# Kernel optimization log

Hardware: AMD Instinct MI355X
Metric: run time of the kernel (lower is better)

Reference implementation:

```python
import jax, jax.numpy as jnp
import numpy as np

N, E, F_IN = 50000, 800000, 128
H, C, CLS, G = 8, 32, 16, 64
NEG_SLOPE = 0.2


def setup_inputs() -> dict:
    key = jax.random.key(0)
    ks = jax.random.split(key, 11)
    s = 0.05
    return {
        "x": jax.random.normal(ks[0], (N, F_IN), jnp.float32),
        "edge_index": jax.random.randint(ks[1], (2, E), 0, N, jnp.int32),
        "batch": jnp.sort(jax.random.randint(ks[2], (N,), 0, G, jnp.int32)),
        "W1": jax.random.normal(ks[3], (F_IN, H * C), jnp.float32) * s,
        "a1_src": jax.random.normal(ks[4], (H, C), jnp.float32) * s,
        "a1_dst": jax.random.normal(ks[5], (H, C), jnp.float32) * s,
        "b1": jax.random.normal(ks[6], (H * C,), jnp.float32) * s,
        "W2": jax.random.normal(ks[7], (H * C, CLS), jnp.float32) * s,
        "a2_src": jax.random.normal(ks[8], (1, CLS), jnp.float32) * s,
        "a2_dst": jax.random.normal(ks[9], (1, CLS), jnp.float32) * s,
        "b2": jax.random.normal(ks[10], (CLS,), jnp.float32) * s,
    }


def _gat_conv(x, src, dst, W, a_s, a_d, b, concat):
    n = x.shape[0]
    Hh, Cc = a_s.shape
    xp = (x @ W).reshape(n, Hh, Cc)                      # [N,H,C]
    al_s = jnp.einsum("nhc,hc->nh", xp, a_s)             # [N,H]
    al_d = jnp.einsum("nhc,hc->nh", xp, a_d)
    e = jax.nn.leaky_relu(al_s[src] + al_d[dst], NEG_SLOPE)  # [E,H]
    m = jax.ops.segment_max(e, dst, num_segments=n)      # segment softmax over dst
    ex = jnp.exp(e - m[dst])
    denom = jax.ops.segment_sum(ex, dst, num_segments=n)
    alpha = ex / denom[dst]                              # [E,H]
    out = jax.ops.segment_sum(xp[src] * alpha[:, :, None], dst, num_segments=n)
    out = out.reshape(n, Hh * Cc) if concat else out.mean(axis=1)
    return out + b


def reference(x, edge_index, batch, W1, a1_src, a1_dst, b1, W2, a2_src, a2_dst, b2):
    n = x.shape[0]
    loops = jnp.arange(n, dtype=edge_index.dtype)        # PyG add_self_loops=True
    ei = jnp.concatenate([edge_index, jnp.stack([loops, loops])], axis=1)
    src, dst = ei[0], ei[1]
    h = jax.nn.elu(_gat_conv(x, src, dst, W1, a1_src, a1_dst, b1, True))
    h = _gat_conv(h, src, dst, W2, a2_src, a2_dst, b2, False)
    counts = jax.ops.segment_sum(jnp.ones((n,), h.dtype), batch, num_segments=G)
    pooled = jax.ops.segment_sum(h, batch, num_segments=G) / jnp.maximum(counts, 1.0)[:, None]
    return jax.nn.log_softmax(pooled, axis=1)
```

## Files before the change

kernel.cpp:

```cpp
#include <hip/hip_runtime.h>
#include <math.h>

#define N_NODES 50000
#define N_EDGES 800000
#define FDIM 128
#define NH 8
#define NC 32
#define D1 256
#define NCLS 16
#define NGRP 64
#define NEG 0.2f
#define E_TOT (N_EDGES + N_NODES)
#define NB_N 196
#define G1_BLOCKS 782
#define E_CHUNK 4096
#define NCHUNK 196
#define NBIN 196

typedef __attribute__((ext_vector_type(8))) unsigned short u16x8;
typedef __attribute__((ext_vector_type(4))) unsigned short u16x4;
typedef __attribute__((ext_vector_type(8))) short short8;
typedef __attribute__((ext_vector_type(4))) float f32x4;

static __device__ __forceinline__ float bf2f(unsigned short u) {
    return __uint_as_float(((unsigned int)u) << 16);
}
static __device__ __forceinline__ unsigned short f2bf(float f) {
    unsigned int b = __float_as_uint(f);
    return (unsigned short)((b + 0x7FFFu + ((b >> 16) & 1u)) >> 16);
}

__global__ __launch_bounds__(256) void k_init(
    const float* __restrict__ W1, unsigned short* __restrict__ w1p,
    float* __restrict__ poolS, float* __restrict__ poolC,
    const int* __restrict__ ei, int* __restrict__ binmat) {
    __shared__ int h[NBIN];
    int c = blockIdx.x;
    for (int b = threadIdx.x; b < NBIN; b += 256) h[b] = 0;
    __syncthreads();
    int e0 = c * E_CHUNK;
    int e1 = e0 + E_CHUNK; if (e1 > N_EDGES) e1 = N_EDGES;
    for (int e = e0 + threadIdx.x; e < e1; e += 256)
        atomicAdd(&h[ei[N_EDGES + e] >> 8], 1);
    int i = blockIdx.x * 256 + threadIdx.x;
    if (i < NGRP * NCLS) poolS[i] = 0.f;
    if (i < NGRP) poolC[i] = 0.f;
    if (i < FDIM * D1) {
        int ks = i >> 13;
        int r = i & 8191;
        int nt2 = r >> 9;
        int r2 = r & 511;
        int lane = r2 >> 3, e = r2 & 7;
        int k = ks * 32 + (lane >> 4) * 8 + e;
        int col = nt2 * 16 + (lane & 15);
        w1p[i] = f2bf(W1[k * D1 + col]);
    }
    __syncthreads();
    for (int b = threadIdx.x; b < NBIN; b += 256) binmat[b * NCHUNK + c] = h[b];
}

__global__ __launch_bounds__(256) void k_binprescan(int* __restrict__ binmat,
                                                    int* __restrict__ binTot) {
    __shared__ int sh[256];
    int b = blockIdx.x, t = threadIdx.x;
    int v = (t < NCHUNK) ? binmat[b * NCHUNK + t] : 0;
    sh[t] = v;
    __syncthreads();
    for (int d = 1; d < 256; d <<= 1) {
        int tv = (t >= d) ? sh[t - d] : 0;
        __syncthreads();
        sh[t] += tv;
        __syncthreads();
    }
    if (t < NCHUNK) binmat[b * NCHUNK + t] = sh[t] - v;
    if (t == 255) binTot[b] = sh[255];
}

__global__ __launch_bounds__(256) void k_basescan(const int* __restrict__ binTot,
                                                  int* __restrict__ binBase) {
    __shared__ int sh[256];
    int t = threadIdx.x;
    int v = (t < NBIN) ? binTot[t] : 0;
    sh[t] = v;
    __syncthreads();
    for (int d = 1; d < 256; d <<= 1) {
        int tv = (t >= d) ? sh[t - d] : 0;
        __syncthreads();
        sh[t] += tv;
        __syncthreads();
    }
    if (t < NBIN) binBase[t] = sh[t] - v;
}

__global__ __launch_bounds__(256) void k_gemm1m(
    const float* __restrict__ x, const unsigned short* __restrict__ w1p,
    const float* __restrict__ a1s, const float* __restrict__ a1d,
    unsigned short* __restrict__ xp1b, float* __restrict__ al1s,
    float* __restrict__ al1d) {
    const int l = threadIdx.x & 63;
    const int wid = threadIdx.x >> 6;
    const int wr = wid >> 1, wc = wid & 1;
    const int l15 = l & 15, l4 = l >> 4;
    const int base = blockIdx.x * 64;
    const int r0 = base + wr * 32;

    f32x4 acc[2][8] = {};
#pragma unroll
    for (int ks = 0; ks < 4; ++ks) {
        const int kk = ks * 32 + l4 * 8;
        short8 af[2];
#pragma unroll
        for (int rt = 0; rt < 2; ++rt) {
            int row = r0 + rt * 16 + l15;
            float4 v0 = make_float4(0.f, 0.f, 0.f, 0.f), v1 = v0;
            if (row < N_NODES) {
                const float* xr = x + (size_t)row * FDIM + kk;
                v0 = *(const float4*)xr;
                v1 = *(const float4*)(xr + 4);
            }
            short8 a;
            a[0] = (short)f2bf(v0.x); a[1] = (short)f2bf(v0.y);
            a[2] = (short)f2bf(v0.z); a[3] = (short)f2bf(v0.w);
            a[4] = (short)f2bf(v1.x); a[5] = (short)f2bf(v1.y);
            a[6] = (short)f2bf(v1.z); a[7] = (short)f2bf(v1.w);
            af[rt] = a;
        }
#pragma unroll
        for (int nt = 0; nt < 8; ++nt) {
            int nt2 = wc * 8 + nt;
            short8 bf_ = *(const short8*)&w1p[(size_t)((ks * 16 + nt2) * 64 + l) * 8];
            acc[0][nt] = __builtin_amdgcn_mfma_f32_16x16x32_bf16(af[0], bf_, acc[0][nt], 0, 0, 0);
            acc[1][nt] = __builtin_amdgcn_mfma_f32_16x16x32_bf16(af[1], bf_, acc[1][nt], 0, 0, 0);
        }
    }
#pragma unroll
    for (int rt = 0; rt < 2; ++rt) {
        int rbase = r0 + rt * 16 + l4 * 4;
#pragma unroll
        for (int nt = 0; nt < 8; ++nt) {
            int col = wc * 128 + nt * 16 + l15;
            f32x4 c = acc[rt][nt];
#pragma unroll
            for (int r = 0; r < 4; ++r) {
                int row = rbase + r;
                if (row < N_NODES) xp1b[(size_t)row * D1 + col] = f2bf(c[r]);
            }
        }
    }
#pragma unroll
    for (int hl = 0; hl < 4; ++hl) {
        int hg = wc * 4 + hl;
        float as0 = a1s[hg * NC + l15], as1 = a1s[hg * NC + 16 + l15];
        float ad0 = a1d[hg * NC + l15], ad1 = a1d[hg * NC + 16 + l15];
#pragma unroll
        for (int rt = 0; rt < 2; ++rt) {
            f32x4 c0 = acc[rt][2 * hl], c1 = acc[rt][2 * hl + 1];
#pragma unroll
            for (int r = 0; r < 4; ++r) {
                float ss = c0[r] * as0 + c1[r] * as1;
                float dd = c0[r] * ad0 + c1[r] * ad1;
#pragma unroll
                for (int msk = 1; msk < 16; msk <<= 1) {
                    ss += __shfl_xor(ss, msk);
                    dd += __shfl_xor(dd, msk);
                }
                int row = r0 + rt * 16 + l4 * 4 + r;
                if (l15 == 0 && row < N_NODES) {
                    al1s[row * NH + hg] = ss;
                    al1d[row * NH + hg] = dd;
                }
            }
        }
    }
}

__global__ __launch_bounds__(256) void k_binscatter(const int* __restrict__ ei,
                                                    const int* __restrict__ offs,
                                                    const int* __restrict__ binBase,
                                                    int* __restrict__ binned) {
    __shared__ int cur[NBIN];
    int c = blockIdx.x;
    for (int b = threadIdx.x; b < NBIN; b += 256)
        cur[b] = binBase[b] + offs[b * NCHUNK + c];
    __syncthreads();
    int e0 = c * E_CHUNK;
    int e1 = e0 + E_CHUNK; if (e1 > N_EDGES) e1 = N_EDGES;
    for (int e = e0 + threadIdx.x; e < e1; e += 256) {
        int s = ei[e], d = ei[N_EDGES + e];
        int pos = atomicAdd(&cur[d >> 8], 1);
        binned[pos] = s | ((d & 255) << 16);
    }
}

__global__ __launch_bounds__(256) void k_bincsr(const int* __restrict__ binBase,
                                                const int* __restrict__ binned,
                                                int* __restrict__ rowptr,
                                                int* __restrict__ cnt,
                                                int* __restrict__ esrc) {
    __shared__ int lcnt[256];
    __shared__ int sh[256];
    __shared__ int lcur[256];
    int b = blockIdx.x;
    int t = threadIdx.x;
    int estart = binBase[b];
    int eend = (b == NBIN - 1) ? N_EDGES : binBase[b + 1];
    int nbase = b * 256;
    int nin = N_NODES - nbase; if (nin > 256) nin = 256;
    lcnt[t] = 0;
    __syncthreads();
    for (int e = estart + t; e < eend; e += 256)
        atomicAdd(&lcnt[(binned[e] >> 16) & 255], 1);
    __syncthreads();
    int myc = lcnt[t] + (t < nin ? 1 : 0);
    sh[t] = myc;
    __syncthreads();
    for (int d = 1; d < 256; d <<= 1) {
        int v = (t >= d) ? sh[t - d] : 0;
        __syncthreads();
        sh[t] += v;
        __syncthreads();
    }
    int excl = sh[t] - myc;
    int outbase = estart + nbase;
    int rp = outbase + excl;
    if (t < nin) {
        rowptr[nbase + t] = rp;
        cnt[nbase + t] = myc;
        esrc[rp] = nbase + t;
    }
    lcur[t] = rp + (t < nin ? 1 : 0);
    __syncthreads();
    for (int e = estart + t; e < eend; e += 256) {
        int v = binned[e];
        int pos = atomicAdd(&lcur[(v >> 16) & 255], 1);
        esrc[pos] = v & 0xFFFF;
    }
}

__global__ __launch_bounds__(256) void k_att1(
    const unsigned short* __restrict__ xp1b, const float* __restrict__ al1s,
    const float* __restrict__ al1d, const float* __restrict__ b1,
    const int* __restrict__ rowptr, const int* __restrict__ cnt,
    const int* __restrict__ esrc, unsigned short* __restrict__ h1b) {
    __shared__ int s_src[4][64];
    __shared__ float s_alpha[4][64 * 8];
    int wv = threadIdx.x >> 6;
    int lane = threadIdx.x & 63;
    int n = blockIdx.x * 4 + wv;
    int start = rowptr[n];
    int deg = cnt[n];
    int dcap = deg < 64 ? deg : 64;
    for (int j = lane; j < dcap; j += 64) s_src[wv][j] = esrc[start + j];
    int h = lane & 7, eg = lane >> 3;
    float ald = al1d[n * NH + h];
    float m = -1e30f, den = 0.f;
    for (int j = eg; j < dcap; j += 8) {
        int s = s_src[wv][j];
        float v = al1s[s * NH + h] + ald;
        v = v > 0.f ? v : NEG * v;
        s_alpha[wv][j * 8 + h] = v;
        if (v > m) { den = den * __expf(m - v) + 1.f; m = v; }
        else den += __expf(v - m);
    }
    for (int j = 64 + eg; j < deg; j += 8) {
        int s = esrc[start + j];
        float v = al1s[s * NH + h] + ald;
        v = v > 0.f ? v : NEG * v;
        if (v > m) { den = den * __expf(m - v) + 1.f; m = v; }
        else den += __expf(v - m);
    }
    for (int msk = 8; msk < 64; msk <<= 1) {
        float mo = __shfl_xor(m, msk), dn = __shfl_xor(den, msk);
        float nm = fmaxf(m, mo);
        den = den * __expf(m - nm) + dn * __expf(mo - nm);
        m = nm;
    }
    float rden1 = 1.f / den;
    for (int j = eg; j < dcap; j += 8) {
        float v = s_alpha[wv][j * 8 + h];
        s_alpha[wv][j * 8 + h] = __expf(v - m) * rden1;
    }
    int hh = lane >> 3;
    int cb = lane << 2;
    float m2 = __shfl(m, hh);
    float rd2 = __shfl(rden1, hh);
    float ald2 = al1d[n * NH + hh];
    float a0 = 0.f, a1 = 0.f, a2 = 0.f, a3 = 0.f;
    for (int j0 = 0; j0 < dcap; j0 += 8) {
        const unsigned short* p[8];
        float aw[8];
#pragma unroll
        for (int k = 0; k < 8; ++k) {
            int e = j0 + k;
            bool act = e < dcap;
            int ee = act ? e : 0;
            int s = s_src[wv][ee];
            aw[k] = act ? s_alpha[wv][ee * 8 + hh] : 0.f;
            p[k] = xp1b + (size_t)s * D1 + cb;
        }
#pragma unroll
        for (int k = 0; k < 8; ++k) {
            u16x4 xv = *(const u16x4*)p[k];
            a0 = fmaf(aw[k], bf2f(xv[0]), a0);
            a1 = fmaf(aw[k], bf2f(xv[1]), a1);
            a2 = fmaf(aw[k], bf2f(xv[2]), a2);
            a3 = fmaf(aw[k], bf2f(xv[3]), a3);
        }
    }
    for (int j = 64; j < deg; ++j) {
        int s = esrc[start + j];
        float v = al1s[s * NH + hh] + ald2;
        v = v > 0.f ? v : NEG * v;
        float al = __expf(v - m2) * rd2;
        u16x4 xv = *(const u16x4*)(xp1b + (size_t)s * D1 + cb);
        a0 = fmaf(al, bf2f(xv[0]), a0);
        a1 = fmaf(al, bf2f(xv[1]), a1);
        a2 = fmaf(al, bf2f(xv[2]), a2);
        a3 = fmaf(al, bf2f(xv[3]), a3);
    }
    float4 bb = *(const float4*)(b1 + cb);
    a0 += bb.x; a1 += bb.y; a2 += bb.z; a3 += bb.w;
    a0 = a0 > 0.f ? a0 : expm1f(a0);
    a1 = a1 > 0.f ? a1 : expm1f(a1);
    a2 = a2 > 0.f ? a2 : expm1f(a2);
    a3 = a3 > 0.f ? a3 : expm1f(a3);
    u16x4 pk = { f2bf(a0), f2bf(a1), f2bf(a2), f2bf(a3) };
    *(u16x4*)(h1b + (size_t)n * D1 + cb) = pk;
}

__global__ __launch_bounds__(256) void k_gemm2(
    const unsigned short* __restrict__ h1b, const float* __restrict__ W2,
    const float* __restrict__ a2s, const float* __restrict__ a2d,
    float* __restrict__ xp2, float* __restrict__ al2s, float* __restrict__ al2d) {
    __shared__ float w2s[D1 * NCLS];
    for (int i = threadIdx.x; i < D1 * NCLS; i += 256) w2s[i] = W2[i];
    __syncthreads();
    int n = blockIdx.x * 256 + threadIdx.x;
    if (n >= N_NODES) return;
    float4 acc[4];
#pragma unroll
    for (int q = 0; q < 4; ++q) acc[q] = make_float4(0.f, 0.f, 0.f, 0.f);
    const unsigned short* hr = h1b + (size_t)n * D1;
    for (int k0 = 0; k0 < D1; k0 += 8) {
        u16x8 hv = *(const u16x8*)(hr + k0);
#pragma unroll
        for (int j = 0; j < 8; ++j) {
            float hx = bf2f(hv[j]);
#pragma unroll
            for (int q = 0; q < 4; ++q) {
                float4 w = *(const float4*)(&w2s[(k0 + j) * NCLS + q * 4]);
                acc[q].x = fmaf(hx, w.x, acc[q].x);
                acc[q].y = fmaf(hx, w.y, acc[q].y);
                acc[q].z = fmaf(hx, w.z, acc[q].z);
                acc[q].w = fmaf(hx, w.w, acc[q].w);
            }
        }
    }
    float ss = 0.f, dd = 0.f;
#pragma unroll
    for (int q = 0; q < 4; ++q) {
        *(float4*)(xp2 + (size_t)n * NCLS + q * 4) = acc[q];
        float4 s4 = *(const float4*)(a2s + q * 4);
        float4 d4 = *(const float4*)(a2d + q * 4);
        ss += acc[q].x * s4.x + acc[q].y * s4.y + acc[q].z * s4.z + acc[q].w * s4.w;
        dd += acc[q].x * d4.x + acc[q].y * d4.y + acc[q].z * d4.z + acc[q].w * d4.w;
    }
    al2s[n] = ss;
    al2d[n] = dd;
}

__global__ __launch_bounds__(256) void k_att2(
    const float* __restrict__ xp2, const float* __restrict__ al2s,
    const float* __restrict__ al2d, const float* __restrict__ b2,
    const int* __restrict__ rowptr, const int* __restrict__ cnt,
    const int* __restrict__ esrc, float* __restrict__ out2) {
    __shared__ int s_src[4][64];
    __shared__ float s_a[4][64];
    int wave = threadIdx.x >> 6;
    int lane = threadIdx.x & 63;
    int n = blockIdx.x * 4 + wave;
    int start = rowptr[n];
    int deg = cnt[n];
    int dcap = deg < 64 ? deg : 64;
    float ald = al2d[n];
    float m = -1e30f, den = 0.f;
    for (int j = lane; j < dcap; j += 64) {
        int s = esrc[start + j];
        s_src[wave][j] = s;
        float v = al2s[s] + ald;
        v = v > 0.f ? v : NEG * v;
        s_a[wave][j] = v;
        if (v > m) { den = den * __expf(m - v) + 1.f; m = v; }
        else den += __expf(v - m);
    }
    for (int j = 64 + lane; j < deg; j += 64) {
        float v = al2s[esrc[start + j]] + ald;
        v = v > 0.f ? v : NEG * v;
        if (v > m) { den = den * __expf(m - v) + 1.f; m = v; }
        else den += __expf(v - m);
    }
    for (int msk = 1; msk < 64; msk <<= 1) {
        float mo = __shfl_xor(m, msk), dn = __shfl_xor(den, msk);
        float nm = fmaxf(m, mo);
        den = den * __expf(m - nm) + dn * __expf(mo - nm);
        m = nm;
    }
    float rden = 1.f / den;
    for (int j = lane; j < dcap; j += 64)
        s_a[wave][j] = __expf(s_a[wave][j] - m) * rden;
    int c = lane & 15;
    int eg = lane >> 4;
    float acc = 0.f;
    for (int j0 = 0; j0 < dcap; j0 += 8) {
        const float* p[2];
        float aw[2];
#pragma unroll
        for (int k = 0; k < 2; ++k) {
            int e = j0 + eg + 4 * k;
            bool act = e < dcap;
            int ee = act ? e : 0;
            aw[k] = act ? s_a[wave][ee] : 0.f;
            p[k] = xp2 + (size_t)s_src[wave][ee] * NCLS + c;
        }
        acc = fmaf(aw[0], p[0][0], acc);
        acc = fmaf(aw[1], p[1][0], acc);
    }
    for (int j = 64 + eg; j < deg; j += 4) {
        int s = esrc[start + j];
        float v = al2s[s] + ald;
        v = v > 0.f ? v : NEG * v;
        acc += __expf(v - m) * rden * xp2[(size_t)s * NCLS + c];
    }
    acc += __shfl_xor(acc, 16);
    acc += __shfl_xor(acc, 32);
    if (lane < 16) out2[(size_t)n * NCLS + lane] = acc + b2[lane];
}

__global__ __launch_bounds__(256) void k_pool(
    const float* __restrict__ out2, const int* __restrict__ batch,
    float* __restrict__ poolS, float* __restrict__ poolC) {
    __shared__ float sacc[NGRP * NCLS];
    __shared__ float scnt[NGRP];
    for (int i = threadIdx.x; i < NGRP * NCLS; i += 256) sacc[i] = 0.f;
    if (threadIdx.x < NGRP) scnt[threadIdx.x] = 0.f;
    __syncthreads();
    int n = blockIdx.x * 256 + threadIdx.x;
    if (n < N_NODES) {
        int g = batch[n];
        atomicAdd(&scnt[g], 1.f);
#pragma unroll
        for (int q = 0; q < 4; ++q) {
            float4 v = *(const float4*)(out2 + (size_t)n * NCLS + q * 4);
            atomicAdd(&sacc[g * NCLS + q * 4 + 0], v.x);
            atomicAdd(&sacc[g * NCLS + q * 4 + 1], v.y);
            atomicAdd(&sacc[g * NCLS + q * 4 + 2], v.z);
            atomicAdd(&sacc[g * NCLS + q * 4 + 3], v.w);
        }
    }
    __syncthreads();
    for (int i = threadIdx.x; i < NGRP * NCLS; i += 256)
        if (sacc[i] != 0.f) atomicAdd(&poolS[i], sacc[i]);
    if (threadIdx.x < NGRP && scnt[threadIdx.x] != 0.f)
        atomicAdd(&poolC[threadIdx.x], scnt[threadIdx.x]);
}

__global__ void k_final(const float* __restrict__ poolS,
                        const float* __restrict__ poolC, float* __restrict__ out) {
    int g = threadIdx.x;
    if (g >= NGRP) return;
    float inv = 1.f / fmaxf(poolC[g], 1.f);
    float v[NCLS];
    float m = -1e30f;
#pragma unroll
    for (int c = 0; c < NCLS; ++c) {
        v[c] = poolS[g * NCLS + c] * inv;
        m = fmaxf(m, v[c]);
    }
    float s = 0.f;
#pragma unroll
    for (int c = 0; c < NCLS; ++c) s += expf(v[c] - m);
    float lse = m + logf(s);
#pragma unroll
    for (int c = 0; c < NCLS; ++c) out[g * NCLS + c] = v[c] - lse;
}

extern "C" void kernel_launch(void* const* d_in, const int* in_sizes, int n_in,
                              void* d_out, int out_size, void* d_ws, size_t ws_size,
                              hipStream_t stream) {
    const float* x    = (const float*)d_in[0];
    const int*   ei   = (const int*)d_in[1];
    const int*   batch = (const int*)d_in[2];
    const float* W1   = (const float*)d_in[3];
    const float* a1s  = (const float*)d_in[4];
    const float* a1d  = (const float*)d_in[5];
    const float* b1   = (const float*)d_in[6];
    const float* W2   = (const float*)d_in[7];
    const float* a2s  = (const float*)d_in[8];
    const float* a2d  = (const float*)d_in[9];
    const float* b2   = (const float*)d_in[10];
    float* out = (float*)d_out;

    float* f = (float*)d_ws;
    float* al1s_ = f;  f += (size_t)N_NODES * NH;
    float* al1d_ = f;  f += (size_t)N_NODES * NH;
    float* xp2   = f;  f += (size_t)N_NODES * NCLS;
    float* al2s_ = f;  f += N_NODES;
    float* al2d_ = f;  f += N_NODES;
    float* out2  = f;  f += (size_t)N_NODES * NCLS;
    float* poolS = f;  f += NGRP * NCLS;
    float* poolC = f;  f += NGRP;
    unsigned short* xp1b = (unsigned short*)f;
    unsigned short* h1b  = xp1b + (size_t)N_NODES * D1;
    unsigned short* w1p  = h1b + (size_t)N_NODES * D1;
    int* binmat  = (int*)(w1p + FDIM * D1);
    int* binTot  = binmat + NBIN * NCHUNK;
    int* binBase = binTot + NBIN;
    int* binned  = binBase + NBIN;
    int* rowptr  = binned + N_EDGES;
    int* cnt     = rowptr + N_NODES;
    int* esrc    = cnt + N_NODES;

    k_init<<<NB_N, 256, 0, stream>>>(W1, w1p, poolS, poolC, ei, binmat);
    k_binprescan<<<NBIN, 256, 0, stream>>>(binmat, binTot);
    k_basescan<<<1, 256, 0, stream>>>(binTot, binBase);
    k_gemm1m<<<G1_BLOCKS, 256, 0, stream>>>(x, w1p, a1s, a1d, xp1b, al1s_, al1d_);
    k_binscatter<<<NCHUNK, 256, 0, stream>>>(ei, binmat, binBase, binned);
    k_bincsr<<<NBIN, 256, 0, stream>>>(binBase, binned, rowptr, cnt, esrc);
    k_att1<<<N_NODES / 4, 256, 0, stream>>>(xp1b, al1s_, al1d_, b1, rowptr, cnt, esrc, h1b);
    k_gemm2<<<NB_N, 256, 0, stream>>>(h1b, W2, a2s, a2d, xp2, al2s_, al2d_);
    k_att2<<<N_NODES / 4, 256, 0, stream>>>(xp2, al2s_, al2d_, b2, rowptr, cnt, esrc, out2);
    k_pool<<<NB_N, 256, 0, stream>>>(out2, batch, poolS, poolC);
    k_final<<<1, 64, 0, stream>>>(poolS, poolC, out);
}
```

Baseline: 193.4 us.

## Fold base scan into consumers, two-pass softmax, padded gather loops, deferred normalization

Removes the single-block k_basescan launch by having k_binscatter and k_bincsr recompute the bin prefix scan redundantly in each block. In both attention kernels, the online softmax with per-step exp rescaling is replaced by a max pass then a sum pass. Division by the denominator is moved to the end, multiplied once into the output. Neighbor lists are padded to multiples of 8 with zero weights so the gather loops drop bounds checks, and 32-bit shifted offsets replace size_t pointer math. The cost is an extra esrc/al1s reread for nodes with degree above 64, plus redundant scan work in every bin block.

```diff
diff --git a/kernel.cpp b/kernel.cpp
--- a/kernel.cpp
+++ b/kernel.cpp
@@ -76,22 +76,6 @@
     if (t == 255) binTot[b] = sh[255];
 }
 
-__global__ __launch_bounds__(256) void k_basescan(const int* __restrict__ binTot,
-                                                  int* __restrict__ binBase) {
-    __shared__ int sh[256];
-    int t = threadIdx.x;
-    int v = (t < NBIN) ? binTot[t] : 0;
-    sh[t] = v;
-    __syncthreads();
-    for (int d = 1; d < 256; d <<= 1) {
-        int tv = (t >= d) ? sh[t - d] : 0;
-        __syncthreads();
-        sh[t] += tv;
-        __syncthreads();
-    }
-    if (t < NBIN) binBase[t] = sh[t] - v;
-}
-
 __global__ __launch_bounds__(256) void k_gemm1m(
     const float* __restrict__ x, const unsigned short* __restrict__ w1p,
     const float* __restrict__ a1s, const float* __restrict__ a1d,
@@ -176,34 +160,54 @@
 
 __global__ __launch_bounds__(256) void k_binscatter(const int* __restrict__ ei,
                                                     const int* __restrict__ offs,
-                                                    const int* __restrict__ binBase,
+                                                    const int* __restrict__ binTot,
                                                     int* __restrict__ binned) {
     __shared__ int cur[NBIN];
+    __shared__ int sb[256];
     int c = blockIdx.x;
-    for (int b = threadIdx.x; b < NBIN; b += 256)
-        cur[b] = binBase[b] + offs[b * NCHUNK + c];
+    int t = threadIdx.x;
+    int v = (t < NBIN) ? binTot[t] : 0;
+    sb[t] = v;
+    __syncthreads();
+    for (int d = 1; d < 256; d <<= 1) {
+        int tv = (t >= d) ? sb[t - d] : 0;
+        __syncthreads();
+        sb[t] += tv;
+        __syncthreads();
+    }
+    if (t < NBIN) cur[t] = (sb[t] - v) + offs[t * NCHUNK + c];
     __syncthreads();
     int e0 = c * E_CHUNK;
     int e1 = e0 + E_CHUNK; if (e1 > N_EDGES) e1 = N_EDGES;
-    for (int e = e0 + threadIdx.x; e < e1; e += 256) {
+    for (int e = e0 + t; e < e1; e += 256) {
         int s = ei[e], d = ei[N_EDGES + e];
         int pos = atomicAdd(&cur[d >> 8], 1);
         binned[pos] = s | ((d & 255) << 16);
     }
 }
 
-__global__ __launch_bounds__(256) void k_bincsr(const int* __restrict__ binBase,
+__global__ __launch_bounds__(256) void k_bincsr(const int* __restrict__ binTot,
                                                 const int* __restrict__ binned,
                                                 int* __restrict__ rowptr,
                                                 int* __restrict__ cnt,
                                                 int* __restrict__ esrc) {
+    __shared__ int sh[256];
     __shared__ int lcnt[256];
-    __shared__ int sh[256];
     __shared__ int lcur[256];
     int b = blockIdx.x;
     int t = threadIdx.x;
-    int estart = binBase[b];
-    int eend = (b == NBIN - 1) ? N_EDGES : binBase[b + 1];
+    int v = (t < NBIN) ? binTot[t] : 0;
+    sh[t] = v;
+    __syncthreads();
+    for (int d = 1; d < 256; d <<= 1) {
+        int tv = (t >= d) ? sh[t - d] : 0;
+        __syncthreads();
+        sh[t] += tv;
+        __syncthreads();
+    }
+    int estart = (b == 0) ? 0 : sh[b - 1];
+    int eend = sh[b];
+    __syncthreads();
     int nbase = b * 256;
     int nin = N_NODES - nbase; if (nin > 256) nin = 256;
     lcnt[t] = 0;
@@ -215,9 +219,9 @@
     sh[t] = myc;
     __syncthreads();
     for (int d = 1; d < 256; d <<= 1) {
-        int v = (t >= d) ? sh[t - d] : 0;
-        __syncthreads();
-        sh[t] += v;
+        int tv = (t >= d) ? sh[t - d] : 0;
+        __syncthreads();
+        sh[t] += tv;
         __syncthreads();
     }
     int excl = sh[t] - myc;
@@ -231,9 +235,9 @@
     lcur[t] = rp + (t < nin ? 1 : 0);
     __syncthreads();
     for (int e = estart + t; e < eend; e += 256) {
-        int v = binned[e];
-        int pos = atomicAdd(&lcur[(v >> 16) & 255], 1);
-        esrc[pos] = v & 0xFFFF;
+        int vv = binned[e];
+        int pos = atomicAdd(&lcur[(vv >> 16) & 255], 1);
+        esrc[pos] = vv & 0xFFFF;
     }
 }
 
@@ -250,76 +254,87 @@
     int start = rowptr[n];
     int deg = cnt[n];
     int dcap = deg < 64 ? deg : 64;
-    for (int j = lane; j < dcap; j += 64) s_src[wv][j] = esrc[start + j];
+    int dpad = (dcap + 7) & ~7;
+    for (int j = lane; j < dpad; j += 64)
+        s_src[wv][j] = (j < dcap) ? esrc[start + j] : n;
+    int npad = (dpad - dcap) * 8;
+    if (lane < npad) s_alpha[wv][dcap * 8 + lane] = 0.f;
     int h = lane & 7, eg = lane >> 3;
     float ald = al1d[n * NH + h];
-    float m = -1e30f, den = 0.f;
+    float m = -1e30f;
     for (int j = eg; j < dcap; j += 8) {
         int s = s_src[wv][j];
         float v = al1s[s * NH + h] + ald;
-        v = v > 0.f ? v : NEG * v;
+        v = fmaxf(v, NEG * v);
         s_alpha[wv][j * 8 + h] = v;
-        if (v > m) { den = den * __expf(m - v) + 1.f; m = v; }
-        else den += __expf(v - m);
-    }
-    for (int j = 64 + eg; j < deg; j += 8) {
-        int s = esrc[start + j];
-        float v = al1s[s * NH + h] + ald;
-        v = v > 0.f ? v : NEG * v;
-        if (v > m) { den = den * __expf(m - v) + 1.f; m = v; }
-        else den += __expf(v - m);
-    }
-    for (int msk = 8; msk < 64; msk <<= 1) {
-        float mo = __shfl_xor(m, msk), dn = __shfl_xor(den, msk);
-        float nm = fmaxf(m, mo);
-        den = den * __expf(m - nm) + dn * __expf(mo - nm);
-        m = nm;
-    }
-    float rden1 = 1.f / den;
+        m = fmaxf(m, v);
+    }
+    if (deg > 64) {
+        for (int j = 64 + eg; j < deg; j += 8) {
+            int s = esrc[start + j];
+            float v = al1s[s * NH + h] + ald;
+            m = fmaxf(m, fmaxf(v, NEG * v));
+        }
+    }
+    for (int msk = 8; msk < 64; msk <<= 1) m = fmaxf(m, __shfl_xor(m, msk));
+    float den = 0.f;
     for (int j = eg; j < dcap; j += 8) {
-        float v = s_alpha[wv][j * 8 + h];
-        s_alpha[wv][j * 8 + h] = __expf(v - m) * rden1;
-    }
+        float e = __expf(s_alpha[wv][j * 8 + h] - m);
+        s_alpha[wv][j * 8 + h] = e;
+        den += e;
+    }
+    if (deg > 64) {
+        for (int j = 64 + eg; j < deg; j += 8) {
+            int s = esrc[start + j];
+            float v = al1s[s * NH + h] + ald;
+            v = fmaxf(v, NEG * v);
+            den += __expf(v - m);
+        }
+    }
+    for (int msk = 8; msk < 64; msk <<= 1) den += __shfl_xor(den, msk);
     int hh = lane >> 3;
-    int cb = lane << 2;
+    int cbb = lane << 3;
+    float rd2 = 1.f / __shfl(den, hh);
     float m2 = __shfl(m, hh);
-    float rd2 = __shfl(rden1, hh);
-    float ald2 = al1d[n * NH + hh];
     float a0 = 0.f, a1 = 0.f, a2 = 0.f, a3 = 0.f;
-    for (int j0 = 0; j0 < dcap; j0 += 8) {
-        const unsigned short* p[8];
+    for (int j0 = 0; j0 < dpad; j0 += 8) {
+        int off[8];
         float aw[8];
 #pragma unroll
         for (int k = 0; k < 8; ++k) {
-            int e = j0 + k;
-            bool act = e < dcap;
-            int ee = act ? e : 0;
-            int s = s_src[wv][ee];
-            aw[k] = act ? s_alpha[wv][ee * 8 + hh] : 0.f;
-            p[k] = xp1b + (size_t)s * D1 + cb;
+            int s = s_src[wv][j0 + k];
+            aw[k] = s_alpha[wv][(j0 + k) * 8 + hh];
+            off[k] = (s << 9) + cbb;
         }
 #pragma unroll
         for (int k = 0; k < 8; ++k) {
-            u16x4 xv = *(const u16x4*)p[k];
+            u16x4 xv = *(const u16x4*)((const char*)xp1b + off[k]);
             a0 = fmaf(aw[k], bf2f(xv[0]), a0);
             a1 = fmaf(aw[k], bf2f(xv[1]), a1);
             a2 = fmaf(aw[k], bf2f(xv[2]), a2);
             a3 = fmaf(aw[k], bf2f(xv[3]), a3);
         }
     }
-    for (int j = 64; j < deg; ++j) {
-        int s = esrc[start + j];
-        float v = al1s[s * NH + hh] + ald2;
-        v = v > 0.f ? v : NEG * v;
-        float al = __expf(v - m2) * rd2;
-        u16x4 xv = *(const u16x4*)(xp1b + (size_t)s * D1 + cb);
-        a0 = fmaf(al, bf2f(xv[0]), a0);
-        a1 = fmaf(al, bf2f(xv[1]), a1);
-        a2 = fmaf(al, bf2f(xv[2]), a2);
-        a3 = fmaf(al, bf2f(xv[3]), a3);
-    }
+    if (deg > 64) {
+        float ald2 = al1d[n * NH + hh];
+        for (int j = 64; j < deg; ++j) {
+            int s = esrc[start + j];
+            float v = al1s[s * NH + hh] + ald2;
+            v = fmaxf(v, NEG * v);
+            float al = __expf(v - m2);
+            u16x4 xv = *(const u16x4*)((const char*)xp1b + (s << 9) + cbb);
+            a0 = fmaf(al, bf2f(xv[0]), a0);
+            a1 = fmaf(al, bf2f(xv[1]), a1);
+            a2 = fmaf(al, bf2f(xv[2]), a2);
+            a3 = fmaf(al, bf2f(xv[3]), a3);
+        }
+    }
+    int cb = lane << 2;
     float4 bb = *(const float4*)(b1 + cb);
-    a0 += bb.x; a1 += bb.y; a2 += bb.z; a3 += bb.w;
+    a0 = fmaf(a0, rd2, bb.x);
+    a1 = fmaf(a1, rd2, bb.y);
+    a2 = fmaf(a2, rd2, bb.z);
+    a3 = fmaf(a3, rd2, bb.w);
     a0 = a0 > 0.f ? a0 : expm1f(a0);
     a1 = a1 > 0.f ? a1 : expm1f(a1);
     a2 = a2 > 0.f ? a2 : expm1f(a2);
@@ -382,58 +397,64 @@
     int start = rowptr[n];
     int deg = cnt[n];
     int dcap = deg < 64 ? deg : 64;
+    int dpad = (dcap + 7) & ~7;
+    for (int j = lane; j < dpad; j += 64)
+        s_src[wave][j] = (j < dcap) ? esrc[start + j] : n;
+    if (lane < dpad - dcap) s_a[wave][dcap + lane] = 0.f;
     float ald = al2d[n];
-    float m = -1e30f, den = 0.f;
+    float m = -1e30f;
     for (int j = lane; j < dcap; j += 64) {
-        int s = esrc[start + j];
-        s_src[wave][j] = s;
+        int s = s_src[wave][j];
         float v = al2s[s] + ald;
-        v = v > 0.f ? v : NEG * v;
+        v = fmaxf(v, NEG * v);
         s_a[wave][j] = v;
-        if (v > m) { den = den * __expf(m - v) + 1.f; m = v; }
-        else den += __expf(v - m);
-    }
-    for (int j = 64 + lane; j < deg; j += 64) {
-        float v = al2s[esrc[start + j]] + ald;
-        v = v > 0.f ? v : NEG * v;
-        if (v > m) { den = den * __expf(m - v) + 1.f; m = v; }
-        else den += __expf(v - m);
-    }
-    for (int msk = 1; msk < 64; msk <<= 1) {
-        float mo = __shfl_xor(m, msk), dn = __shfl_xor(den, msk);
-        float nm = fmaxf(m, mo);
-        den = den * __expf(m - nm) + dn * __expf(mo - nm);
-        m = nm;
-    }
+        m = fmaxf(m, v);
+    }
+    if (deg > 64) {
+        for (int j = 64 + lane; j < deg; j += 64) {
+            float v = al2s[esrc[start + j]] + ald;
+            m = fmaxf(m, fmaxf(v, NEG * v));
+        }
+    }
+    for (int msk = 1; msk < 64; msk <<= 1) m = fmaxf(m, __shfl_xor(m, msk));
+    float den = 0.f;
+    for (int j = lane; j < dcap; j += 64) {
+        float e = __expf(s_a[wave][j] - m);
+        s_a[wave][j] = e;
+        den += e;
+    }
+    if (deg > 64) {
+        for (int j = 64 + lane; j < deg; j += 64) {
+            float v = al2s[esrc[start + j]] + ald;
+            v = fmaxf(v, NEG * v);
+            den += __expf(v - m);
+        }
+    }
+    for (int msk = 1; msk < 64; msk <<= 1) den += __shfl_xor(den, msk);
     float rden = 1.f / den;
-    for (int j = lane; j < dcap; j += 64)
-        s_a[wave][j] = __expf(s_a[wave][j] - m) * rden;
     int c = lane & 15;
     int eg = lane >> 4;
     float acc = 0.f;
-    for (int j0 = 0; j0 < dcap; j0 += 8) {
-        const float* p[2];
-        float aw[2];
+    for (int j0 = 0; j0 < dpad; j0 += 8) {
 #pragma unroll
         for (int k = 0; k < 2; ++k) {
             int e = j0 + eg + 4 * k;
-            bool act = e < dcap;
-            int ee = act ? e : 0;
-            aw[k] = act ? s_a[wave][ee] : 0.f;
-            p[k] = xp2 + (size_t)s_src[wave][ee] * NCLS + c;
-        }
-        acc = fmaf(aw[0], p[0][0], acc);
-        acc = fmaf(aw[1], p[1][0], acc);
-    }
-    for (int j = 64 + eg; j < deg; j += 4) {
-        int s = esrc[start + j];
-        float v = al2s[s] + ald;
-        v = v > 0.f ? v : NEG * v;
-        acc += __expf(v - m) * rden * xp2[(size_t)s * NCLS + c];
+            float aw = s_a[wave][e];
+            int s = s_src[wave][e];
+            acc = fmaf(aw, xp2[(size_t)s * NCLS + c], acc);
+        }
+    }
+    if (deg > 64) {
+        for (int j = 64 + eg; j < deg; j += 4) {
+            int s = esrc[start + j];
+            float v = al2s[s] + ald;
+            v = fmaxf(v, NEG * v);
+            acc += __expf(v - m) * xp2[(size_t)s * NCLS + c];
+        }
     }
     acc += __shfl_xor(acc, 16);
     acc += __shfl_xor(acc, 32);
-    if (lane < 16) out2[(size_t)n * NCLS + lane] = acc + b2[lane];
+    if (lane < 16) out2[(size_t)n * NCLS + lane] = acc * rden + b2[lane];
 }
 
 __global__ __launch_bounds__(256) void k_pool(
@@ -514,18 +535,16 @@
     unsigned short* w1p  = h1b + (size_t)N_NODES * D1;
     int* binmat  = (int*)(w1p + FDIM * D1);
     int* binTot  = binmat + NBIN * NCHUNK;
-    int* binBase = binTot + NBIN;
-    int* binned  = binBase + NBIN;
+    int* binned  = binTot + NBIN;
     int* rowptr  = binned + N_EDGES;
     int* cnt     = rowptr + N_NODES;
     int* esrc    = cnt + N_NODES;
 
     k_init<<<NB_N, 256, 0, stream>>>(W1, w1p, poolS, poolC, ei, binmat);
     k_binprescan<<<NBIN, 256, 0, stream>>>(binmat, binTot);
-    k_basescan<<<1, 256, 0, stream>>>(binTot, binBase);
     k_gemm1m<<<G1_BLOCKS, 256, 0, stream>>>(x, w1p, a1s, a1d, xp1b, al1s_, al1d_);
-    k_binscatter<<<NCHUNK, 256, 0, stream>>>(ei, binmat, binBase, binned);
-    k_bincsr<<<NBIN, 256, 0, stream>>>(binBase, binned, rowptr, cnt, esrc);
+    k_binscatter<<<NCHUNK, 256, 0, stream>>>(ei, binmat, binTot, binned);
+    k_bincsr<<<NBIN, 256, 0, stream>>>(binTot, binned, rowptr, cnt, esrc);
     k_att1<<<N_NODES / 4, 256, 0, stream>>>(xp1b, al1s_, al1d_, b1, rowptr, cnt, esrc, h1b);
     k_gemm2<<<NB_N, 256, 0, stream>>>(h1b, W2, a2s, a2d, xp2, al2s_, al2d_);
     k_att2<<<N_NODES / 4, 256, 0, stream>>>(xp2, al2s_, al2d_, b2, rowptr, cnt, esrc, out2);
```

Measured after the change: 192.7 us. About the same (-0.4%).
